# Kernel tuning notes

Hardware: AMD Instinct MI355X
Metric: run time of the kernel (lower is better)

Reference implementation:

```python
import jax, jax.numpy as jnp
import numpy as np

NEG = -1.0e30  # log-space 'zero' that is safe in fp32
EPS = 1e-7     # keras.backend.ctc_batch_cost epsilon


def setup_inputs() -> dict:
    key = jax.random.key(0)
    k1, k2 = jax.random.split(key)
    B, T, C, L = 256, 512, 256, 128
    # y_pred are post-softmax probabilities, as expected by ctc_batch_cost
    logits = jax.random.normal(k1, (B, T, C), dtype=jnp.float32)
    y_pred = jax.nn.softmax(logits, axis=-1)
    # labels in [0, C-1): never equal to blank index C-1
    y_true = jax.random.randint(k2, (B, L), 0, C - 1, dtype=jnp.int32)
    return {"y_true": y_true, "y_pred": y_pred}


def _ctc_batch_cost(y_true, y_pred):
    """Faithful keras.backend.ctc_batch_cost with full input/label lengths.

    y_true: [B, L] int labels (no blanks). y_pred: [B, T, C] probabilities.
    Blank index = C - 1 (TF v1 ctc_loss convention). Returns [B, 1] loss.
    """
    B, T, C = y_pred.shape
    L = y_true.shape[1]
    blank = C - 1
    S = 2 * L + 1  # extended label: blank, l0, blank, l1, ..., blank

    logp = jnp.log(y_pred + EPS)                                # [B, T, C]
    ext = jnp.full((B, S), blank, dtype=y_true.dtype).at[:, 1::2].set(y_true)
    # per-(t, s) log prob of the extended symbol
    lp = jnp.take_along_axis(logp, ext[:, None, :].astype(jnp.int32), axis=2)  # [B, T, S]

    # skip transition s-2 -> s allowed iff s >= 2, ext[s] != blank, ext[s] != ext[s-2]
    ext_m2 = jnp.pad(ext, ((0, 0), (2, 0)), constant_values=blank)[:, :S]
    skip = (ext != blank) & (ext != ext_m2) & (jnp.arange(S)[None, :] >= 2)

    # alpha init at t=0: only s=0 (blank) and s=1 (first label) reachable
    alpha0 = jnp.where(jnp.arange(S)[None, :] < 2, lp[:, 0, :], NEG)  # [B, S]

    def step(alpha, lp_t):
        p1 = jnp.pad(alpha, ((0, 0), (1, 0)), constant_values=NEG)[:, :S]
        p2 = jnp.pad(alpha, ((0, 0), (2, 0)), constant_values=NEG)[:, :S]
        a = jnp.logaddexp(alpha, p1)
        a = jnp.logaddexp(a, jnp.where(skip, p2, NEG))
        return a + lp_t, None

    lp_time_major = jnp.moveaxis(lp, 1, 0)  # [T, B, S]
    alpha, _ = jax.lax.scan(step, alpha0, lp_time_major[1:])
    # total log-likelihood ends at last blank or last label
    loss = -jnp.logaddexp(alpha[:, S - 1], alpha[:, S - 2])    # [B]
    return loss[:, None]                                        # [B, 1]


def reference(y_true, y_pred):
    # CTCLayer.call computes ctc_batch_cost with input_length = T, label_length = L
    # for every batch row, adds it as a loss, and passes y_pred through. The
    # compute of interest is the loss itself, returned here as [B, 1].
    return _ctc_batch_cost(y_true, y_pred)
```

## Files before the change

kernel.cpp:

```cpp
#include <hip/hip_runtime.h>
#include <math.h>


namespace {
constexpr int Bn = 256;
constexpr int Tn = 512;
constexpr int Cn = 256;
constexpr int Ln = 128;
constexpr int D  = 32;
constexpr float EPSf = 1e-7f;
constexpr float LN2f = 0.69314718055994530942f;
constexpr int   TGT  = 100;
}

typedef float f4 __attribute__((ext_vector_type(4)));

#define GLOAD(dst, p) \
    asm volatile("global_load_dwordx4 %0, %1, off" : "=v"(dst) : "v"(p))
#define WAITP(dst) \
    asm volatile("s_waitcnt vmcnt(31)" : "+v"(dst))
#define WAIT0(dst) \
    asm volatile("s_waitcnt vmcnt(0)" : "+v"(dst))

__device__ __forceinline__ float rdl63(float v) {
    return __int_as_float(__builtin_amdgcn_readlane(__float_as_int(v), 63));
}
__device__ __forceinline__ float dpp_shr1(float v) {
    return __int_as_float(__builtin_amdgcn_update_dpp(
        0, __float_as_int(v), 0x138, 0xF, 0xF, true));
}
template <int CTRL>
__device__ __forceinline__ float dpp_max(float m) {
    float o = __int_as_float(__builtin_amdgcn_update_dpp(
        0, __float_as_int(m), CTRL, 0xF, 0xF, true));
    return fmaxf(m, o);
}

__global__ __launch_bounds__(64, 1)
void ctc_fwd(const int* __restrict__ y_true,
             const float* __restrict__ y_pred,
             float* __restrict__ out)
{
    const int b    = blockIdx.x;
    const int lane = threadIdx.x;

    __shared__ __align__(16) float lds[4 * Cn];

    const int* yt = y_true + b * Ln;
    const int l0 = yt[2 * lane];
    const int l1 = yt[2 * lane + 1];
    const int lm = (lane > 0) ? yt[2 * lane - 1] : -1;
    const float sk1 = (lane > 0 && l0 != lm) ? 1.0f : 0.0f;
    const float sk3 = (l1 != l0) ? 1.0f : 0.0f;

    float a0 = (lane == 0) ? 0x1p100f : 0.0f;
    float a1 = 0.0f, a2 = 0.0f, a3 = 0.0f, a4 = 0.0f;
    int Eacc = -100;

    auto step = [&](float rb, float r0, float r1) {
        const float n = dpp_shr1(a3);
        const float Pb = rb + EPSf;
        const float P0 = r0 + EPSf;
        const float P1 = r1 + EPSf;
        const float na0 = (a0 + n) * Pb;
        const float na1 = fmaf(sk1, n,  a1 + a0) * P0;
        const float na2 = (a2 + a1) * Pb;
        const float na3 = fmaf(sk3, a1, a3 + a2) * P1;
        const float na4 = (a4 + a3) * Pb;
        a0 = na0; a1 = na1; a2 = na2; a3 = na3; a4 = na4;
    };

    auto rescale = [&]() {
        float m = fmaxf(fmaxf(fmaxf(a0, a1), fmaxf(a2, a3)), a4);
        m = dpp_max<0x111>(m);
        m = dpp_max<0x112>(m);
        m = dpp_max<0x114>(m);
        m = dpp_max<0x118>(m);
        m = dpp_max<0x142>(m);
        m = dpp_max<0x143>(m);
        m = rdl63(m);
        int e;
        (void)frexpf(m, &e);
        const int shift = TGT - e;
        a0 = ldexpf(a0, shift);
        a1 = ldexpf(a1, shift);
        a2 = ldexpf(a2, shift);
        a3 = ldexpf(a3, shift);
        a4 = ldexpf(a4, shift);
        Eacc -= shift;
    };

    const f4* p = (const f4*)(y_pred + (size_t)b * Tn * Cn) + lane;
    f4 buf[D];
    #pragma unroll
    for (int j = 0; j < D; ++j) { GLOAD(buf[j], p); p += Cn / 4; }

    float bq0 = 0.0f, bq1 = 0.0f;
    float r0c = 0.0f, r1c = 0.0f;

    #pragma unroll
    for (int j = 0; j < D; ++j) {
        WAITP(buf[j]);
        const float bnew = rdl63(buf[j].w);
        float r0n = 0.0f, r1n = 0.0f;
        if (j >= 1) {
            r0n = lds[((j - 1) & 3) * Cn + l0];
            r1n = lds[((j - 1) & 3) * Cn + l1];
        }
        ((f4*)lds)[(j & 3) * (Cn / 4) + lane] = buf[j];
        GLOAD(buf[j], p); p += Cn / 4;
        if (j >= 2) step(bq0, r0c, r1c);
        bq0 = bq1; bq1 = bnew; r0c = r0n; r1c = r1n;
        if (j == 17) rescale();
    }

    for (int c = D; c < Tn - D; c += D) {
        #pragma unroll
        for (int j = 0; j < D; ++j) {
            WAITP(buf[j]);
            const float bnew = rdl63(buf[j].w);
            const float r0n = lds[((j - 1) & 3) * Cn + l0];
            const float r1n = lds[((j - 1) & 3) * Cn + l1];
            ((f4*)lds)[(j & 3) * (Cn / 4) + lane] = buf[j];
            GLOAD(buf[j], p); p += Cn / 4;
            step(bq0, r0c, r1c);
            bq0 = bq1; bq1 = bnew; r0c = r0n; r1c = r1n;
            if (j == 1 || j == 17) rescale();
        }
    }

    #pragma unroll
    for (int j = 0; j < D; ++j) {
        WAIT0(buf[j]);
        const float bnew = rdl63(buf[j].w);
        const float r0n = lds[((j - 1) & 3) * Cn + l0];
        const float r1n = lds[((j - 1) & 3) * Cn + l1];
        ((f4*)lds)[(j & 3) * (Cn / 4) + lane] = buf[j];
        step(bq0, r0c, r1c);
        bq0 = bq1; bq1 = bnew; r0c = r0n; r1c = r1n;
        if (j == 1 || j == 17) rescale();
    }

    {
        const float r0n = lds[3 * Cn + l0];
        const float r1n = lds[3 * Cn + l1];
        step(bq0, r0c, r1c);
        bq0 = bq1; r0c = r0n; r1c = r1n;
        step(bq0, r0c, r1c);
    }

    if (lane == 63) {
        const float s = a3 + a4;
        out[b] = -LN2f * (log2f(s) + (float)Eacc);
    }
}

extern "C" void kernel_launch(void* const* d_in, const int* in_sizes, int n_in,
                              void* d_out, int out_size, void* d_ws, size_t ws_size,
                              hipStream_t stream) {
    const int*   y_true = (const int*)  d_in[0];
    const float* y_pred = (const float*)d_in[1];
    float* out = (float*)d_out;
    (void)in_sizes; (void)n_in; (void)out_size; (void)d_ws; (void)ws_size;
    ctc_fwd<<<dim3(Bn), dim3(64), 0, stream>>>(y_true, y_pred, out);
}
```

Before: 197.8 us.

## Split CTC kernel into loader waves and a single recurrence wave over an LDS ring

The block grows from one wave to eight. Seven producer waves load 32-timestep chunks of y_pred into a 64-slot LDS ring, double-buffered across block barriers. Wave 0 only runs the alpha recurrence, reading the label and blank probabilities from LDS instead of doing its own global loads, waits and readlanes. The goal is to take global-load latency and issue overhead off the serial recurrence chain, at the cost of a block-wide barrier every 32 steps and a larger LDS footprint.

```diff
diff --git a/kernel.cpp b/kernel.cpp
--- a/kernel.cpp
+++ b/kernel.cpp
@@ -7,7 +7,9 @@
 constexpr int Tn = 512;
 constexpr int Cn = 256;
 constexpr int Ln = 128;
-constexpr int D  = 32;
+constexpr int CH = 32;
+constexpr int NCHUNK = Tn / CH;
+constexpr int SLOTS = 64;
 constexpr float EPSf = 1e-7f;
 constexpr float LN2f = 0.69314718055994530942f;
 constexpr int   TGT  = 100;
@@ -17,10 +19,8 @@
 
 #define GLOAD(dst, p) \
     asm volatile("global_load_dwordx4 %0, %1, off" : "=v"(dst) : "v"(p))
-#define WAITP(dst) \
-    asm volatile("s_waitcnt vmcnt(31)" : "+v"(dst))
-#define WAIT0(dst) \
-    asm volatile("s_waitcnt vmcnt(0)" : "+v"(dst))
+#define VMWAIT0() \
+    asm volatile("s_waitcnt vmcnt(0)" ::: "memory")
 
 __device__ __forceinline__ float rdl63(float v) {
     return __int_as_float(__builtin_amdgcn_readlane(__float_as_int(v), 63));
@@ -36,15 +36,37 @@
     return fmaxf(m, o);
 }
 
-__global__ __launch_bounds__(64, 1)
+__global__ __launch_bounds__(512, 1)
 void ctc_fwd(const int* __restrict__ y_true,
              const float* __restrict__ y_pred,
              float* __restrict__ out)
 {
     const int b    = blockIdx.x;
-    const int lane = threadIdx.x;
+    const int tid  = (int)threadIdx.x;
+    const int w    = tid >> 6;
+    const int lane = tid & 63;
 
-    __shared__ __align__(16) float lds[4 * Cn];
+    __shared__ __align__(16) float lds[SLOTS * Cn];
+
+    const f4* gbase = (const f4*)(y_pred + (size_t)b * Tn * Cn);
+    f4* ringv = (f4*)lds;
+
+    auto load_chunk = [&](int ch) {
+        f4 tmp[5];
+        int rows[5];
+        #pragma unroll
+        for (int k = 0; k < 5; ++k) {
+            int rl = (w - 1) + 7 * k;
+            rl = rl > CH - 1 ? CH - 1 : rl;
+            const int t = ch * CH + rl;
+            rows[k] = t;
+            GLOAD(tmp[k], gbase + (size_t)t * (Cn / 4) + lane);
+        }
+        VMWAIT0();
+        #pragma unroll
+        for (int k = 0; k < 5; ++k)
+            ringv[(rows[k] & (SLOTS - 1)) * (Cn / 4) + lane] = tmp[k];
+    };
 
     const int* yt = y_true + b * Ln;
     const int l0 = yt[2 * lane];
@@ -90,68 +112,42 @@
         Eacc -= shift;
     };
 
-    const f4* p = (const f4*)(y_pred + (size_t)b * Tn * Cn) + lane;
-    f4 buf[D];
-    #pragma unroll
-    for (int j = 0; j < D; ++j) { GLOAD(buf[j], p); p += Cn / 4; }
+    auto consume_chunk = [&](int c) {
+        const int t0 = c * CH;
+        int s = (t0 & (SLOTS - 1)) * Cn;
+        float rba = lds[s + (Cn - 1)], r0a = lds[s + l0], r1a = lds[s + l1];
+        s = ((t0 + 1) & (SLOTS - 1)) * Cn;
+        float rbb = lds[s + (Cn - 1)], r0b = lds[s + l0], r1b = lds[s + l1];
+        #pragma unroll
+        for (int j = 0; j < CH; ++j) {
+            float rbn = 0.0f, r0n = 0.0f, r1n = 0.0f;
+            if (j < CH - 2) {
+                const int ss = ((t0 + j + 2) & (SLOTS - 1)) * Cn;
+                rbn = lds[ss + (Cn - 1)];
+                r0n = lds[ss + l0];
+                r1n = lds[ss + l1];
+            }
+            step(rba, r0a, r1a);
+            rba = rbb; r0a = r0b; r1a = r1b;
+            rbb = rbn; r0b = r0n; r1b = r1n;
+            if ((j & 15) == 15) rescale();
+        }
+    };
 
-    float bq0 = 0.0f, bq1 = 0.0f;
-    float r0c = 0.0f, r1c = 0.0f;
-
-    #pragma unroll
-    for (int j = 0; j < D; ++j) {
-        WAITP(buf[j]);
-        const float bnew = rdl63(buf[j].w);
-        float r0n = 0.0f, r1n = 0.0f;
-        if (j >= 1) {
-            r0n = lds[((j - 1) & 3) * Cn + l0];
-            r1n = lds[((j - 1) & 3) * Cn + l1];
+    if (w > 0) load_chunk(0);
+    __syncthreads();
+    for (int c = 0; c < NCHUNK; ++c) {
+        if (w > 0) {
+            if (c + 1 < NCHUNK) load_chunk(c + 1);
+        } else {
+            consume_chunk(c);
         }
-        ((f4*)lds)[(j & 3) * (Cn / 4) + lane] = buf[j];
-        GLOAD(buf[j], p); p += Cn / 4;
-        if (j >= 2) step(bq0, r0c, r1c);
-        bq0 = bq1; bq1 = bnew; r0c = r0n; r1c = r1n;
-        if (j == 17) rescale();
+        __syncthreads();
     }
 
-    for (int c = D; c < Tn - D; c += D) {
-        #pragma unroll
-        for (int j = 0; j < D; ++j) {
-            WAITP(buf[j]);
-            const float bnew = rdl63(buf[j].w);
-            const float r0n = lds[((j - 1) & 3) * Cn + l0];
-            const float r1n = lds[((j - 1) & 3) * Cn + l1];
-            ((f4*)lds)[(j & 3) * (Cn / 4) + lane] = buf[j];
-            GLOAD(buf[j], p); p += Cn / 4;
-            step(bq0, r0c, r1c);
-            bq0 = bq1; bq1 = bnew; r0c = r0n; r1c = r1n;
-            if (j == 1 || j == 17) rescale();
-        }
-    }
-
-    #pragma unroll
-    for (int j = 0; j < D; ++j) {
-        WAIT0(buf[j]);
-        const float bnew = rdl63(buf[j].w);
-        const float r0n = lds[((j - 1) & 3) * Cn + l0];
-        const float r1n = lds[((j - 1) & 3) * Cn + l1];
-        ((f4*)lds)[(j & 3) * (Cn / 4) + lane] = buf[j];
-        step(bq0, r0c, r1c);
-        bq0 = bq1; bq1 = bnew; r0c = r0n; r1c = r1n;
-        if (j == 1 || j == 17) rescale();
-    }
-
-    {
-        const float r0n = lds[3 * Cn + l0];
-        const float r1n = lds[3 * Cn + l1];
-        step(bq0, r0c, r1c);
-        bq0 = bq1; r0c = r0n; r1c = r1n;
-        step(bq0, r0c, r1c);
-    }
-
-    if (lane == 63) {
-        const float s = a3 + a4;
-        out[b] = -LN2f * (log2f(s) + (float)Eacc);
+    if (w == 0 && lane == 63) {
+        const float sfin = a3 + a4;
+        out[b] = -LN2f * (log2f(sfin) + (float)Eacc);
     }
 }
 
@@ -162,5 +158,5 @@
     const float* y_pred = (const float*)d_in[1];
     float* out = (float*)d_out;
     (void)in_sizes; (void)n_in; (void)out_size; (void)d_ws; (void)ws_size;
-    ctc_fwd<<<dim3(Bn), dim3(64), 0, stream>>>(y_true, y_pred, out);
+    ctc_fwd<<<dim3(Bn), dim3(512), 0, stream>>>(y_true, y_pred, out);
 }
```

Measured after the change: 196.4 us. About the same (-0.7%).
